# Optimization experiments

Hardware: AMD Instinct MI355X
Metric: run time of the kernel (lower is better)

The kernel has to match this reference:

```python
import jax, jax.numpy as jnp
import numpy as np

D_MODEL = 1024
NUM_HEAD = 16
BATCH = 2
SEQ = 2048
NEG_INF = -1e9  # matches masked_fill value in the original


def setup_inputs() -> dict:
    key = jax.random.key(0)
    k1, k2, k3, k4, k5 = jax.random.split(key, 5)
    scale = 1.0 / np.sqrt(D_MODEL)
    return {
        "x": jax.random.normal(k1, (BATCH, SEQ, D_MODEL), dtype=jnp.float32),
        "q_weight": jax.random.normal(k2, (D_MODEL, D_MODEL), dtype=jnp.float32) * scale,
        "k_weight": jax.random.normal(k3, (D_MODEL, D_MODEL), dtype=jnp.float32) * scale,
        "v_weight": jax.random.normal(k4, (D_MODEL, D_MODEL), dtype=jnp.float32) * scale,
        "o_weight": jax.random.normal(k5, (D_MODEL, D_MODEL), dtype=jnp.float32) * scale,
    }


def reference(x, q_weight, k_weight, v_weight, o_weight):
    b, s, d = x.shape
    h = NUM_HEAD
    dh = d // h
    # projections: weight layout is (d_out, d_in)
    q = jnp.einsum('bsd,ed->bse', x, q_weight).reshape(b, s, h, dh).transpose(0, 2, 1, 3)
    k = jnp.einsum('bsd,ed->bse', x, k_weight).reshape(b, s, h, dh).transpose(0, 2, 1, 3)
    v = jnp.einsum('bsd,ed->bse', x, v_weight).reshape(b, s, h, dh).transpose(0, 2, 1, 3)
    scores = jnp.einsum('bhqd,bhkd->bhqk', q, k) / jnp.sqrt(jnp.asarray(dh, x.dtype))
    causal = jnp.triu(jnp.ones((s, s), dtype=bool), k=1)  # True above diagonal -> masked
    scores = jnp.where(causal, jnp.asarray(NEG_INF, x.dtype), scores)
    attn = jax.nn.softmax(scores, axis=-1)
    out = jnp.einsum('bhqk,bhkd->bhqd', attn, v)          # [b,h,s,dh]
    out = out.transpose(0, 2, 1, 3).reshape(b, s, d)       # merge heads
    return jnp.einsum('bse,de->bsd', out, o_weight)
```

## Files before the change

### kernel.cpp

```cpp
#include <hip/hip_runtime.h>

typedef short bhalf8 __attribute__((ext_vector_type(8)));
typedef float floatx4 __attribute__((ext_vector_type(4)));

#define D_MODEL 1024
#define SEQ     2048
#define BATCH   2
#define NHEAD   16
#define DH      64

#define GLDS(g, l) __builtin_amdgcn_global_load_lds( \
    (const __attribute__((address_space(1))) void*)(g), \
    (__attribute__((address_space(3))) void*)(l), 16, 0, 0)

static __device__ __forceinline__ short f2bf(float f) {
    unsigned u = __builtin_bit_cast(unsigned, f);
    u = (u + 0x7fffu + ((u >> 16) & 1u)) >> 16;
    return (short)u;
}
static __device__ __forceinline__ unsigned pack2(float a, float b) {
    return (unsigned)(unsigned short)f2bf(a) | ((unsigned)(unsigned short)f2bf(b) << 16);
}
static __device__ __forceinline__ unsigned cvt_pk_bf16(float lo, float hi) {
    unsigned r;
    asm("v_cvt_pk_bf16_f32 %0, %1, %2" : "=v"(r) : "v"(lo), "v"(hi));
    return r;
}

__global__ __launch_bounds__(256) void cast_all(const float* __restrict__ x,
                                                const float* __restrict__ wq,
                                                const float* __restrict__ wk,
                                                const float* __restrict__ wv,
                                                const float* __restrict__ wo,
                                                short* __restrict__ xb,
                                                short* __restrict__ wall) {
    const int bid = blockIdx.x;
    const float* s;
    short* d;
    int i;
    if (bid < 2048) {
        s = x; d = xb;
        i = (bid * 256 + threadIdx.x) * 8;
    } else {
        const int wb = bid - 2048;
        const int which = wb >> 9;
        s = (which == 0) ? wq : (which == 1) ? wk : (which == 2) ? wv : wo;
        d = wall + (size_t)which * (D_MODEL * D_MODEL);
        i = ((wb & 511) * 256 + threadIdx.x) * 8;
    }
    float4 a = *(const float4*)(s + i);
    float4 b = *(const float4*)(s + i + 4);
    uint4 u = {pack2(a.x, a.y), pack2(a.z, a.w), pack2(b.x, b.y), pack2(b.z, b.w)};
    *(uint4*)(d + i) = u;
}

#define MFMA_BF16 __builtin_amdgcn_mfma_f32_16x16x32_bf16

#define QISSUE(kt, s) do {                                                    \
    char* ab_ = pool + (s) * 16384 + (w * 32) * 64;                           \
    char* bb_ = pool + 49152 + (s) * 16384 + (w * 32) * 64;                   \
    GLDS(Ag + (size_t)(kt) * 32, ab_);                                        \
    GLDS(Ag + (size_t)(kt) * 32 + 16 * 1024, ab_ + 1024);                     \
    GLDS(Wg + (size_t)(kt) * 32, bb_);                                        \
    GLDS(Wg + (size_t)(kt) * 32 + 16 * 1024, bb_ + 1024);                     \
} while (0)

#define QCOMP(s) do {                                                         \
    const short(*As_)[32] = (const short(*)[32])(pool + (s) * 16384);         \
    const short(*Bs_)[32] = (const short(*)[32])(pool + 49152 + (s) * 16384); \
    bhalf8 af_[8], bf_[4];                                                    \
    _Pragma("unroll")                                                         \
    for (int m_ = 0; m_ < 8; ++m_)                                            \
        af_[m_] = *(const bhalf8*)&As_[wr * 128 + m_ * 16 + l16][quad * 8];   \
    _Pragma("unroll")                                                         \
    for (int n_ = 0; n_ < 4; ++n_)                                            \
        bf_[n_] = *(const bhalf8*)&Bs_[wc * 64 + n_ * 16 + l16][quad * 8];    \
    __builtin_amdgcn_s_setprio(1);                                            \
    _Pragma("unroll")                                                         \
    for (int m_ = 0; m_ < 8; ++m_)                                            \
        _Pragma("unroll")                                                     \
        for (int n_ = 0; n_ < 4; ++n_)                                        \
            acc[m_][n_] = MFMA_BF16(af_[m_], bf_[n_], acc[m_][n_], 0, 0, 0);  \
    __builtin_amdgcn_s_setprio(0);                                            \
} while (0)

__global__ __launch_bounds__(512) void gemm_qkv2(const short* __restrict__ A,
                                                 const short* __restrict__ W,
                                                 short* __restrict__ Qo,
                                                 short* __restrict__ Ko,
                                                 short* __restrict__ Vt) {
    __shared__ __align__(16) char pool[98304];
    const int t    = threadIdx.x;
    const int w    = t >> 6, lane = t & 63, quad = lane >> 4, l16 = lane & 15;
    const int wr   = w >> 2, wc = w & 3;
    const int bm   = blockIdx.x * 256;
    const int by   = (int)blockIdx.y;
    const int bn   = by * 256;

    const short* Ag = A + (size_t)(bm + w * 32 + (lane >> 2)) * 1024 + (lane & 3) * 8;
    const short* Wg = W + (size_t)(bn + w * 32 + (lane >> 2)) * 1024 + (lane & 3) * 8;

    floatx4 acc[8][4];
#pragma unroll
    for (int m = 0; m < 8; ++m)
#pragma unroll
        for (int n = 0; n < 4; ++n) {
            floatx4 z = {0.f, 0.f, 0.f, 0.f};
            acc[m][n] = z;
        }

    QISSUE(0, 0);
    QISSUE(1, 1);
    int sc_ = 0, sn_ = 2;
#pragma unroll 1
    for (int kt = 0; kt < 30; ++kt) {
        asm volatile("s_waitcnt vmcnt(4)" ::: "memory");
        __builtin_amdgcn_s_barrier();
        QISSUE(kt + 2, sn_);
        QCOMP(sc_);
        sc_ = (sc_ == 2) ? 0 : sc_ + 1;
        sn_ = (sn_ == 2) ? 0 : sn_ + 1;
    }
    asm volatile("s_waitcnt vmcnt(4)" ::: "memory");
    __builtin_amdgcn_s_barrier();
    QCOMP(sc_);
    sc_ = (sc_ == 2) ? 0 : sc_ + 1;
    asm volatile("s_waitcnt vmcnt(0)" ::: "memory");
    __builtin_amdgcn_s_barrier();
    QCOMP(sc_);

    __syncthreads();
    short (*Ct)[268] = (short(*)[268])pool;
    if (by < 8) {
        short* outp = (by < 4) ? Qo : Ko;
        const int colbase = (by < 4) ? bn : bn - 1024;
        for (int hh = 0; hh < 2; ++hh) {
            if (wr == hh) {
#pragma unroll
                for (int m = 0; m < 8; ++m)
#pragma unroll
                    for (int n = 0; n < 4; ++n)
#pragma unroll
                        for (int g = 0; g < 4; ++g)
                            Ct[m * 16 + quad * 4 + g][wc * 64 + n * 16 + l16] =
                                f2bf(acc[m][n][g]);
            }
            __syncthreads();
            {
                const int r = t >> 2, c0 = (t & 3) * 64;
#pragma unroll
                for (int p = 0; p < 8; ++p)
                    *(uint4*)(outp + (size_t)(bm + hh * 128 + r) * 1024 +
                              colbase + c0 + p * 8) =
                        *(const uint4*)&Ct[r][c0 + p * 8];
            }
            __syncthreads();
        }
    } else {
        const int nbase = bn - 2048;
        for (int hh = 0; hh < 2; ++hh) {
            if ((wc >> 1) == hh) {
#pragma unroll
                for (int m = 0; m < 8; ++m)
#pragma unroll
                    for (int n = 0; n < 4; ++n)
#pragma unroll
                        for (int g = 0; g < 4; ++g)
                            Ct[wc * 64 + n * 16 + l16 - hh * 128]
                              [wr * 128 + m * 16 + quad * 4 + g] =
                                f2bf(acc[m][n][g]);
            }
            __syncthreads();
            {
                const int r = t >> 2, c0 = (t & 3) * 64;
#pragma unroll
                for (int p = 0; p < 8; ++p)
                    *(uint4*)(Vt + (size_t)(nbase + hh * 128 + r) * 4096 +
                              bm + c0 + p * 8) =
                        *(const uint4*)&Ct[r][c0 + p * 8];
            }
            __syncthreads();
        }
    }
}

__global__ __launch_bounds__(256) void gemm_o(const short* __restrict__ A,
                                              const short* __restrict__ W,
                                              float* __restrict__ C) {
    __shared__ __align__(16) char pool[34816];
    short (*As)[64] = (short(*)[64])pool;
    short (*Bs)[64] = (short(*)[64])(pool + 16384);
    const int t    = threadIdx.x;
    const int wave = t >> 6, lane = t & 63, quad = lane >> 4, l16 = lane & 15;
    const int bm = blockIdx.x * 128, bn = blockIdx.y * 64;
    const int qm = (wave >> 1) * 64, qn = (wave & 1) * 32;

    const int lrow = lane >> 3, lcol = (lane & 7) * 8;
    const short* Ag = A + (size_t)(bm + wave * 32 + lrow) * 1024 + lcol;
    const short* Wg = W + (size_t)(bn + wave * 16 + lrow) * 1024 + lcol;
    short* Al = &As[wave * 32][0];
    short* Bl = &Bs[wave * 16][0];

    floatx4 acc[4][2];
#pragma unroll
    for (int i = 0; i < 4; ++i)
#pragma unroll
        for (int j = 0; j < 2; ++j) {
            floatx4 z = {0.f, 0.f, 0.f, 0.f};
            acc[i][j] = z;
        }

    for (int k0 = 0; k0 < 1024; k0 += 64) {
        __syncthreads();
#pragma unroll
        for (int j = 0; j < 4; ++j)
            GLDS(Ag + k0 + (size_t)j * 8 * 1024, Al + j * 8 * 64);
#pragma unroll
        for (int j = 0; j < 2; ++j)
            GLDS(Wg + k0 + (size_t)j * 8 * 1024, Bl + j * 8 * 64);
        __syncthreads();
#pragma unroll
        for (int kk = 0; kk < 64; kk += 32) {
            bhalf8 af[4], bfr[2];
#pragma unroll
            for (int im = 0; im < 4; ++im)
                af[im] = *(const bhalf8*)&As[qm + im * 16 + l16][kk + quad * 8];
#pragma unroll
            for (int jn = 0; jn < 2; ++jn)
                bfr[jn] = *(const bhalf8*)&Bs[qn + jn * 16 + l16][kk + quad * 8];
#pragma unroll
            for (int im = 0; im < 4; ++im)
#pragma unroll
                for (int jn = 0; jn < 2; ++jn)
                    acc[im][jn] = __builtin_amdgcn_mfma_f32_16x16x32_bf16(
                        af[im], bfr[jn], acc[im][jn], 0, 0, 0);
        }
    }

    __syncthreads();
    float (*Ctf)[68] = (float(*)[68])pool;
#pragma unroll
    for (int im = 0; im < 4; ++im)
#pragma unroll
        for (int jn = 0; jn < 2; ++jn)
#pragma unroll
            for (int g = 0; g < 4; ++g)
                Ctf[qm + im * 16 + quad * 4 + g][qn + jn * 16 + l16] = acc[im][jn][g];
    __syncthreads();
#pragma unroll
    for (int pass = 0; pass < 8; ++pass) {
        const int r = (t >> 4) + pass * 16;
        const int c = (t & 15) * 4;
        float4 u = *(const float4*)&Ctf[r][c];
        *(float4*)(C + (size_t)(bm + r) * 1024 + bn + c) = u;
    }
}


__global__ __launch_bounds__(512) void attn_v16(const short* __restrict__ Qo,
                                                const short* __restrict__ Ko,
                                                const short* __restrict__ Vt,
                                                short* __restrict__ Y) {
    __shared__ __align__(16) char pool[73728];
    short (*Ks)[64][72] = (short(*)[64][72])pool;
    short (*Vs)[64][72] = (short(*)[64][72])(pool + 18432);
    short (*Ps)[32][72] = (short(*)[32][72])(pool + 36864);
    float (*Cmb)[64][44] = (float(*)[64][44])pool;

    const int t    = threadIdx.x;
    const int wave = t >> 6, lane = t & 63, quad = lane >> 4, l16 = lane & 15;
    const int team = t >> 8, wt = wave & 3, tt = t & 255;
    const int bid  = (int)blockIdx.x;
    const int bh   = bid & 31;
    const int qt   = (bid < 256) ? (bid >> 5) : (15 - ((bid - 256) >> 5));
    const int b = bh >> 4, h = bh & 15;
    const int nct   = qt + 1;
    const int kbase = team * nct * 64;

    const short* Qbase = Qo + (size_t)b * SEQ * 1024 + h * 64;
    const short* Kbase = Ko + (size_t)b * SEQ * 1024 + h * 64;
    const short* Vbase = Vt + (size_t)h * 64 * 4096 + (size_t)b * SEQ;

    const int sr = tt >> 2, sc = (tt & 3) * 8;

    const float KS = 0.125f * 1.44269504f;
    const float CB = 12.0f * 1.44269504f;

    const int qw_ = qt * 128 + wt * 32;
    bhalf8 qf[2][2];
#pragma unroll
    for (int im = 0; im < 2; ++im) {
        const short* qr = Qbase + (size_t)(qw_ + im * 16 + l16) * 1024;
        qf[im][0] = *(const bhalf8*)(qr + quad * 8);
        qf[im][1] = *(const bhalf8*)(qr + 32 + quad * 8);
    }

    float lsum[2][4];
    floatx4 o[2][4];
#pragma unroll
    for (int im = 0; im < 2; ++im) {
#pragma unroll
        for (int g = 0; g < 4; ++g) lsum[im][g] = 0.f;
#pragma unroll
        for (int nd = 0; nd < 4; ++nd) {
            floatx4 z = {0.f, 0.f, 0.f, 0.f};
            o[im][nd] = z;
        }
    }

    uint4 kr0, kr1, vr0, vr1;
    kr0 = *(const uint4*)(Kbase + (size_t)(kbase + sr) * 1024 + sc);
    kr1 = *(const uint4*)(Kbase + (size_t)(kbase + sr) * 1024 + sc + 32);
    vr0 = *(const uint4*)(Vbase + (size_t)sr * 4096 + kbase + sc);
    vr1 = *(const uint4*)(Vbase + (size_t)sr * 4096 + kbase + sc + 32);

#pragma unroll 1
    for (int i = 0; i < nct; ++i) {
        __syncthreads();
        *(uint4*)&Ks[team][sr][sc]      = kr0;
        *(uint4*)&Ks[team][sr][sc + 32] = kr1;
        *(uint4*)&Vs[team][sr][sc]      = vr0;
        *(uint4*)&Vs[team][sr][sc + 32] = vr1;
        __syncthreads();
        if (i + 1 < nct) {
            const int kn = kbase + (i + 1) * 64;
            kr0 = *(const uint4*)(Kbase + (size_t)(kn + sr) * 1024 + sc);
            kr1 = *(const uint4*)(Kbase + (size_t)(kn + sr) * 1024 + sc + 32);
            vr0 = *(const uint4*)(Vbase + (size_t)sr * 4096 + kn + sc);
            vr1 = *(const uint4*)(Vbase + (size_t)sr * 4096 + kn + sc + 32);
        }
        const int k0 = kbase + i * 64;
        if (k0 <= qw_ + 31) {
            bhalf8 kf[4][2];
#pragma unroll
            for (int jn = 0; jn < 4; ++jn) {
                kf[jn][0] = *(const bhalf8*)&Ks[team][jn * 16 + l16][quad * 8];
                kf[jn][1] = *(const bhalf8*)&Ks[team][jn * 16 + l16][32 + quad * 8];
            }
            const bool partial = (k0 + 64 > qw_);
#pragma unroll
            for (int im = 0; im < 2; ++im) {
                floatx4 s_[4];
#pragma unroll
                for (int jn = 0; jn < 4; ++jn) {
                    floatx4 z = {0.f, 0.f, 0.f, 0.f};
                    z = MFMA_BF16(qf[im][0], kf[jn][0], z, 0, 0, 0);
                    z = MFMA_BF16(qf[im][1], kf[jn][1], z, 0, 0, 0);
                    s_[jn] = z;
                }
#pragma unroll
                for (int g = 0; g < 4; ++g) {
                    const int rr = im * 16 + quad * 4 + g;
                    const int qrow = qw_ + rr;
                    float e0 = exp2f(s_[0][g] * KS - CB);
                    float e1 = exp2f(s_[1][g] * KS - CB);
                    float e2 = exp2f(s_[2][g] * KS - CB);
                    float e3 = exp2f(s_[3][g] * KS - CB);
                    if (partial) {
                        if (k0 + l16 > qrow)      e0 = 0.f;
                        if (k0 + 16 + l16 > qrow) e1 = 0.f;
                        if (k0 + 32 + l16 > qrow) e2 = 0.f;
                        if (k0 + 48 + l16 > qrow) e3 = 0.f;
                    }
                    lsum[im][g] += (e0 + e1) + (e2 + e3);
                    unsigned r01 = cvt_pk_bf16(e0, e1);
                    unsigned r23 = cvt_pk_bf16(e2, e3);
                    Ps[wave][rr][l16]      = (short)r01;
                    Ps[wave][rr][16 + l16] = (short)(r01 >> 16);
                    Ps[wave][rr][32 + l16] = (short)r23;
                    Ps[wave][rr][48 + l16] = (short)(r23 >> 16);
                }
            }
            bhalf8 vf[4][2];
#pragma unroll
            for (int nd = 0; nd < 4; ++nd) {
                vf[nd][0] = *(const bhalf8*)&Vs[team][nd * 16 + l16][quad * 8];
                vf[nd][1] = *(const bhalf8*)&Vs[team][nd * 16 + l16][32 + quad * 8];
            }
#pragma unroll
            for (int im = 0; im < 2; ++im) {
                bhalf8 ap0 = *(const bhalf8*)&Ps[wave][im * 16 + l16][quad * 8];
                bhalf8 ap1 = *(const bhalf8*)&Ps[wave][im * 16 + l16][32 + quad * 8];
#pragma unroll
                for (int nd = 0; nd < 4; ++nd) {
                    o[im][nd] = MFMA_BF16(ap0, vf[nd][0], o[im][nd], 0, 0, 0);
                    o[im][nd] = MFMA_BF16(ap1, vf[nd][1], o[im][nd], 0, 0, 0);
                }
            }
        }
    }

    __syncthreads();
    if (team == 1) {
        float* cp = &Cmb[wt][lane][0];
#pragma unroll
        for (int im = 0; im < 2; ++im)
#pragma unroll
            for (int nd = 0; nd < 4; ++nd)
                *(floatx4*)(cp + (im * 4 + nd) * 4) = o[im][nd];
#pragma unroll
        for (int im = 0; im < 2; ++im)
#pragma unroll
            for (int g = 0; g < 4; ++g)
                cp[32 + im * 4 + g] = lsum[im][g];
    }
    __syncthreads();
    if (team == 0) {
        const float* cp = &Cmb[wt][lane][0];
#pragma unroll
        for (int im = 0; im < 2; ++im)
#pragma unroll
            for (int nd = 0; nd < 4; ++nd)
                o[im][nd] += *(const floatx4*)(cp + (im * 4 + nd) * 4);
#pragma unroll
        for (int im = 0; im < 2; ++im)
#pragma unroll
            for (int g = 0; g < 4; ++g) {
                float r = lsum[im][g] + cp[32 + im * 4 + g];
                r += __shfl_xor(r, 1, 64);
                r += __shfl_xor(r, 2, 64);
                r += __shfl_xor(r, 4, 64);
                r += __shfl_xor(r, 8, 64);
                const float iv = 1.0f / r;
                const int qrow = qw_ + im * 16 + quad * 4 + g;
#pragma unroll
                for (int nd = 0; nd < 4; ++nd)
                    Y[(size_t)(b * SEQ + qrow) * 1024 + h * 64 + nd * 16 + l16] =
                        f2bf(o[im][nd][g] * iv);
            }
    }
}

extern "C" void kernel_launch(void* const* d_in, const int* in_sizes, int n_in,
                              void* d_out, int out_size, void* d_ws, size_t ws_size,
                              hipStream_t stream) {
    const float* x  = (const float*)d_in[0];
    const float* wq = (const float*)d_in[1];
    const float* wk = (const float*)d_in[2];
    const float* wv = (const float*)d_in[3];
    const float* wo = (const float*)d_in[4];

    short* xb   = (short*)d_ws;
    short* Qo   = xb + (size_t)4096 * 1024;
    short* Ko   = Qo + (size_t)4096 * 1024;
    short* Vt   = Ko + (size_t)4096 * 1024;
    short* wall = Vt + (size_t)1024 * 4096;
    short* wob  = wall + (size_t)3 * 1024 * 1024;

    cast_all<<<dim3(4096), 256, 0, stream>>>(x, wq, wk, wv, wo, xb, wall);
    gemm_qkv2<<<dim3(16, 12), 512, 0, stream>>>(xb, wall, Qo, Ko, Vt);
    attn_v16<<<dim3(512), 512, 0, stream>>>(Qo, Ko, Vt, xb);
    gemm_o<<<dim3(32, 16), 256, 0, stream>>>(xb, wob, (float*)d_out);
}
```

Measured before the change: 190.4 us.

## Restructure attention: per-wave 16-row tiles, register-resident P, double-buffered K/V

The attention kernel changes from two key-split teams of 4 waves, each owning 32 query rows, to 8 waves each owning 16 query rows that walk the whole causal key range. Computing S transposed (K as the A operand) lets the exponentiated probabilities be packed straight into MFMA A-operand registers, which removes the P round trip through shared memory and the cross-team combine step. K/V tiles are double-buffered with one barrier per iteration, and the heavy query tiles are now scheduled first. The trade-off is twice as many sequential key iterations per block, more K/V fragment reloads per wave, and V fragments read as 4-element pieces.

```diff
diff --git a/kernel.cpp b/kernel.cpp
--- a/kernel.cpp
+++ b/kernel.cpp
@@ -1,6 +1,8 @@
 #include <hip/hip_runtime.h>
 
 typedef short bhalf8 __attribute__((ext_vector_type(8)));
+typedef short short4v __attribute__((ext_vector_type(4)));
+typedef unsigned uint4v __attribute__((ext_vector_type(4)));
 typedef float floatx4 __attribute__((ext_vector_type(4)));
 
 #define D_MODEL 1024
@@ -257,177 +259,128 @@
 }
 
 
-__global__ __launch_bounds__(512) void attn_v16(const short* __restrict__ Qo,
+__global__ __launch_bounds__(512) void attn_v17(const short* __restrict__ Qo,
                                                 const short* __restrict__ Ko,
                                                 const short* __restrict__ Vt,
                                                 short* __restrict__ Y) {
-    __shared__ __align__(16) char pool[73728];
-    short (*Ks)[64][72] = (short(*)[64][72])pool;
-    short (*Vs)[64][72] = (short(*)[64][72])(pool + 18432);
-    short (*Ps)[32][72] = (short(*)[32][72])(pool + 36864);
-    float (*Cmb)[64][44] = (float(*)[64][44])pool;
+    __shared__ __align__(16) short Ks[2][64][72];
+    __shared__ __align__(16) short Vs[2][64][72];
 
     const int t    = threadIdx.x;
     const int wave = t >> 6, lane = t & 63, quad = lane >> 4, l16 = lane & 15;
-    const int team = t >> 8, wt = wave & 3, tt = t & 255;
     const int bid  = (int)blockIdx.x;
     const int bh   = bid & 31;
-    const int qt   = (bid < 256) ? (bid >> 5) : (15 - ((bid - 256) >> 5));
+    const int p    = (bid & 255) >> 5;
+    const int qt   = (bid < 256) ? (15 - p) : p;
     const int b = bh >> 4, h = bh & 15;
-    const int nct   = qt + 1;
-    const int kbase = team * nct * 64;
+    const int nc   = (qt + 1) * 2;
 
     const short* Qbase = Qo + (size_t)b * SEQ * 1024 + h * 64;
     const short* Kbase = Ko + (size_t)b * SEQ * 1024 + h * 64;
     const short* Vbase = Vt + (size_t)h * 64 * 4096 + (size_t)b * SEQ;
 
-    const int sr = tt >> 2, sc = (tt & 3) * 8;
+    const int sr = t >> 3;
+    const int sc = (t & 7) * 8;
 
     const float KS = 0.125f * 1.44269504f;
     const float CB = 12.0f * 1.44269504f;
 
-    const int qw_ = qt * 128 + wt * 32;
-    bhalf8 qf[2][2];
-#pragma unroll
-    for (int im = 0; im < 2; ++im) {
-        const short* qr = Qbase + (size_t)(qw_ + im * 16 + l16) * 1024;
-        qf[im][0] = *(const bhalf8*)(qr + quad * 8);
-        qf[im][1] = *(const bhalf8*)(qr + 32 + quad * 8);
-    }
-
-    float lsum[2][4];
-    floatx4 o[2][4];
-#pragma unroll
-    for (int im = 0; im < 2; ++im) {
-#pragma unroll
-        for (int g = 0; g < 4; ++g) lsum[im][g] = 0.f;
-#pragma unroll
-        for (int nd = 0; nd < 4; ++nd) {
-            floatx4 z = {0.f, 0.f, 0.f, 0.f};
-            o[im][nd] = z;
-        }
-    }
-
-    uint4 kr0, kr1, vr0, vr1;
-    kr0 = *(const uint4*)(Kbase + (size_t)(kbase + sr) * 1024 + sc);
-    kr1 = *(const uint4*)(Kbase + (size_t)(kbase + sr) * 1024 + sc + 32);
-    vr0 = *(const uint4*)(Vbase + (size_t)sr * 4096 + kbase + sc);
-    vr1 = *(const uint4*)(Vbase + (size_t)sr * 4096 + kbase + sc + 32);
+    const int qw_  = qt * 128 + wave * 16;
+    const int qrow = qw_ + l16;
+    const short* qr = Qbase + (size_t)qrow * 1024;
+    bhalf8 qf0 = *(const bhalf8*)(qr + quad * 8);
+    bhalf8 qf1 = *(const bhalf8*)(qr + 32 + quad * 8);
+
+    float lsum = 0.f;
+    floatx4 o[4];
+#pragma unroll
+    for (int nd = 0; nd < 4; ++nd) {
+        floatx4 z = {0.f, 0.f, 0.f, 0.f};
+        o[nd] = z;
+    }
+
+    uint4 kreg, vreg;
+    kreg = *(const uint4*)(Kbase + (size_t)sr * 1024 + sc);
+    vreg = *(const uint4*)(Vbase + (size_t)sr * 4096 + sc);
+    *(uint4*)&Ks[0][sr][sc] = kreg;
+    *(uint4*)&Vs[0][sr][sc] = vreg;
+    if (nc > 1) {
+        kreg = *(const uint4*)(Kbase + (size_t)(64 + sr) * 1024 + sc);
+        vreg = *(const uint4*)(Vbase + (size_t)sr * 4096 + 64 + sc);
+    }
+    __syncthreads();
 
 #pragma unroll 1
-    for (int i = 0; i < nct; ++i) {
+    for (int i = 0; i < nc; ++i) {
+        const int buf = i & 1;
+        if (i + 1 < nc) {
+            *(uint4*)&Ks[buf ^ 1][sr][sc] = kreg;
+            *(uint4*)&Vs[buf ^ 1][sr][sc] = vreg;
+        }
+        if (i + 2 < nc) {
+            const int kn = (i + 2) * 64;
+            kreg = *(const uint4*)(Kbase + (size_t)(kn + sr) * 1024 + sc);
+            vreg = *(const uint4*)(Vbase + (size_t)sr * 4096 + kn + sc);
+        }
+        const int k0 = i * 64;
+        if (k0 <= qw_ + 15) {
+            bhalf8 kf[4][2];
+#pragma unroll
+            for (int jn = 0; jn < 4; ++jn) {
+                kf[jn][0] = *(const bhalf8*)&Ks[buf][jn * 16 + l16][quad * 8];
+                kf[jn][1] = *(const bhalf8*)&Ks[buf][jn * 16 + l16][32 + quad * 8];
+            }
+            floatx4 s_[4];
+#pragma unroll
+            for (int jn = 0; jn < 4; ++jn) {
+                floatx4 z = {0.f, 0.f, 0.f, 0.f};
+                z = MFMA_BF16(kf[jn][0], qf0, z, 0, 0, 0);
+                z = MFMA_BF16(kf[jn][1], qf1, z, 0, 0, 0);
+                s_[jn] = z;
+            }
+            const bool partial = (k0 + 64 > qw_);
+            float e[4][4];
+#pragma unroll
+            for (int jn = 0; jn < 4; ++jn)
+#pragma unroll
+                for (int g = 0; g < 4; ++g) {
+                    float v = exp2f(s_[jn][g] * KS - CB);
+                    if (partial && (k0 + jn * 16 + quad * 4 + g > qrow)) v = 0.f;
+                    e[jn][g] = v;
+                    lsum += v;
+                }
+            uint4v w0 = {cvt_pk_bf16(e[0][0], e[0][1]), cvt_pk_bf16(e[0][2], e[0][3]),
+                         cvt_pk_bf16(e[1][0], e[1][1]), cvt_pk_bf16(e[1][2], e[1][3])};
+            uint4v w1 = {cvt_pk_bf16(e[2][0], e[2][1]), cvt_pk_bf16(e[2][2], e[2][3]),
+                         cvt_pk_bf16(e[3][0], e[3][1]), cvt_pk_bf16(e[3][2], e[3][3])};
+            bhalf8 af0 = __builtin_bit_cast(bhalf8, w0);
+            bhalf8 af1 = __builtin_bit_cast(bhalf8, w1);
+#pragma unroll
+            for (int nd = 0; nd < 4; ++nd) {
+                const short* vrow = &Vs[buf][nd * 16 + l16][0];
+                bhalf8 vf0, vf1;
+                *(short4v*)&vf0       = *(const short4v*)(vrow + quad * 4);
+                *((short4v*)&vf0 + 1) = *(const short4v*)(vrow + 16 + quad * 4);
+                *(short4v*)&vf1       = *(const short4v*)(vrow + 32 + quad * 4);
+                *((short4v*)&vf1 + 1) = *(const short4v*)(vrow + 48 + quad * 4);
+                o[nd] = MFMA_BF16(af0, vf0, o[nd], 0, 0, 0);
+                o[nd] = MFMA_BF16(af1, vf1, o[nd], 0, 0, 0);
+            }
+        }
         __syncthreads();
-        *(uint4*)&Ks[team][sr][sc]      = kr0;
-        *(uint4*)&Ks[team][sr][sc + 32] = kr1;
-        *(uint4*)&Vs[team][sr][sc]      = vr0;
-        *(uint4*)&Vs[team][sr][sc + 32] = vr1;
-        __syncthreads();
-        if (i + 1 < nct) {
-            const int kn = kbase + (i + 1) * 64;
-            kr0 = *(const uint4*)(Kbase + (size_t)(kn + sr) * 1024 + sc);
-            kr1 = *(const uint4*)(Kbase + (size_t)(kn + sr) * 1024 + sc + 32);
-            vr0 = *(const uint4*)(Vbase + (size_t)sr * 4096 + kn + sc);
-            vr1 = *(const uint4*)(Vbase + (size_t)sr * 4096 + kn + sc + 32);
-        }
-        const int k0 = kbase + i * 64;
-        if (k0 <= qw_ + 31) {
-            bhalf8 kf[4][2];
-#pragma unroll
-            for (int jn = 0; jn < 4; ++jn) {
-                kf[jn][0] = *(const bhalf8*)&Ks[team][jn * 16 + l16][quad * 8];
-                kf[jn][1] = *(const bhalf8*)&Ks[team][jn * 16 + l16][32 + quad * 8];
-            }
-            const bool partial = (k0 + 64 > qw_);
-#pragma unroll
-            for (int im = 0; im < 2; ++im) {
-                floatx4 s_[4];
-#pragma unroll
-                for (int jn = 0; jn < 4; ++jn) {
-                    floatx4 z = {0.f, 0.f, 0.f, 0.f};
-                    z = MFMA_BF16(qf[im][0], kf[jn][0], z, 0, 0, 0);
-                    z = MFMA_BF16(qf[im][1], kf[jn][1], z, 0, 0, 0);
-                    s_[jn] = z;
-                }
-#pragma unroll
-                for (int g = 0; g < 4; ++g) {
-                    const int rr = im * 16 + quad * 4 + g;
-                    const int qrow = qw_ + rr;
-                    float e0 = exp2f(s_[0][g] * KS - CB);
-                    float e1 = exp2f(s_[1][g] * KS - CB);
-                    float e2 = exp2f(s_[2][g] * KS - CB);
-                    float e3 = exp2f(s_[3][g] * KS - CB);
-                    if (partial) {
-                        if (k0 + l16 > qrow)      e0 = 0.f;
-                        if (k0 + 16 + l16 > qrow) e1 = 0.f;
-                        if (k0 + 32 + l16 > qrow) e2 = 0.f;
-                        if (k0 + 48 + l16 > qrow) e3 = 0.f;
-                    }
-                    lsum[im][g] += (e0 + e1) + (e2 + e3);
-                    unsigned r01 = cvt_pk_bf16(e0, e1);
-                    unsigned r23 = cvt_pk_bf16(e2, e3);
-                    Ps[wave][rr][l16]      = (short)r01;
-                    Ps[wave][rr][16 + l16] = (short)(r01 >> 16);
-                    Ps[wave][rr][32 + l16] = (short)r23;
-                    Ps[wave][rr][48 + l16] = (short)(r23 >> 16);
-                }
-            }
-            bhalf8 vf[4][2];
-#pragma unroll
-            for (int nd = 0; nd < 4; ++nd) {
-                vf[nd][0] = *(const bhalf8*)&Vs[team][nd * 16 + l16][quad * 8];
-                vf[nd][1] = *(const bhalf8*)&Vs[team][nd * 16 + l16][32 + quad * 8];
-            }
-#pragma unroll
-            for (int im = 0; im < 2; ++im) {
-                bhalf8 ap0 = *(const bhalf8*)&Ps[wave][im * 16 + l16][quad * 8];
-                bhalf8 ap1 = *(const bhalf8*)&Ps[wave][im * 16 + l16][32 + quad * 8];
-#pragma unroll
-                for (int nd = 0; nd < 4; ++nd) {
-                    o[im][nd] = MFMA_BF16(ap0, vf[nd][0], o[im][nd], 0, 0, 0);
-                    o[im][nd] = MFMA_BF16(ap1, vf[nd][1], o[im][nd], 0, 0, 0);
-                }
-            }
-        }
-    }
-
-    __syncthreads();
-    if (team == 1) {
-        float* cp = &Cmb[wt][lane][0];
-#pragma unroll
-        for (int im = 0; im < 2; ++im)
-#pragma unroll
-            for (int nd = 0; nd < 4; ++nd)
-                *(floatx4*)(cp + (im * 4 + nd) * 4) = o[im][nd];
-#pragma unroll
-        for (int im = 0; im < 2; ++im)
-#pragma unroll
-            for (int g = 0; g < 4; ++g)
-                cp[32 + im * 4 + g] = lsum[im][g];
-    }
-    __syncthreads();
-    if (team == 0) {
-        const float* cp = &Cmb[wt][lane][0];
-#pragma unroll
-        for (int im = 0; im < 2; ++im)
-#pragma unroll
-            for (int nd = 0; nd < 4; ++nd)
-                o[im][nd] += *(const floatx4*)(cp + (im * 4 + nd) * 4);
-#pragma unroll
-        for (int im = 0; im < 2; ++im)
-#pragma unroll
-            for (int g = 0; g < 4; ++g) {
-                float r = lsum[im][g] + cp[32 + im * 4 + g];
-                r += __shfl_xor(r, 1, 64);
-                r += __shfl_xor(r, 2, 64);
-                r += __shfl_xor(r, 4, 64);
-                r += __shfl_xor(r, 8, 64);
-                const float iv = 1.0f / r;
-                const int qrow = qw_ + im * 16 + quad * 4 + g;
-#pragma unroll
-                for (int nd = 0; nd < 4; ++nd)
-                    Y[(size_t)(b * SEQ + qrow) * 1024 + h * 64 + nd * 16 + l16] =
-                        f2bf(o[im][nd][g] * iv);
-            }
+    }
+
+    lsum += __shfl_xor(lsum, 16, 64);
+    lsum += __shfl_xor(lsum, 32, 64);
+#pragma unroll
+    for (int g = 0; g < 4; ++g) {
+        const float r  = __shfl(lsum, quad * 4 + g, 64);
+        const float iv = 1.0f / r;
+        const int qrow_o = qw_ + quad * 4 + g;
+#pragma unroll
+        for (int nd = 0; nd < 4; ++nd)
+            Y[(size_t)(b * SEQ + qrow_o) * 1024 + h * 64 + nd * 16 + l16] =
+                f2bf(o[nd][g] * iv);
     }
 }
 
@@ -449,6 +402,6 @@
 
     cast_all<<<dim3(4096), 256, 0, stream>>>(x, wq, wk, wv, wo, xb, wall);
     gemm_qkv2<<<dim3(16, 12), 512, 0, stream>>>(xb, wall, Qo, Ko, Vt);
-    attn_v16<<<dim3(512), 512, 0, stream>>>(Qo, Ko, Vt, xb);
+    attn_v17<<<dim3(512), 512, 0, stream>>>(Qo, Ko, Vt, xb);
     gemm_o<<<dim3(32, 16), 256, 0, stream>>>(xb, wob, (float*)d_out);
 }
```

After: 189.5 us. Within noise of the previous version (-0.4%).
